# Kernel tuning notes

Measured on AMD Instinct MI355X. Metric: run time of the kernel, lower is better.

Reference implementation:

```python
import jax, jax.numpy as jnp
import numpy as np

BATCH, N_LABELS, HIDDEN, N_EDGES = 2048, 10000, 768, 20000
PENALTY = 1e-4


def setup_inputs() -> dict:
    key = jax.random.key(0)
    k1, k2, k3, k4, k5 = jax.random.split(key, 5)
    logits = jax.random.normal(k1, (BATCH, N_LABELS), dtype=jnp.float32)
    targets = jax.random.uniform(k2, (BATCH, N_LABELS), dtype=jnp.float32)
    params = jax.random.normal(k3, (N_LABELS, HIDDEN), dtype=jnp.float32)
    parent_idx = jax.random.randint(k4, (N_EDGES,), 0, N_LABELS, dtype=jnp.int32)
    child_idx = jax.random.randint(k5, (N_EDGES,), 0, N_LABELS, dtype=jnp.int32)
    return {"logits": logits, "targets": targets, "params": params,
            "parent_idx": parent_idx, "child_idx": child_idx}


def reference(logits, targets, params, parent_idx, child_idx):
    # BCEWithLogitsLoss (mean reduction): softplus(x) - t*x, numerically stable
    bce = jnp.mean(jax.nn.softplus(logits) - targets * logits)
    # recursive regularization: 0.5 * sum_edges ||param[parent] - param[child]||^2
    diff = params[parent_idx] - params[child_idx]  # [E, H] gather-diff
    reg = 0.5 * jnp.sum(diff * diff)
    return bce + PENALTY * reg
```

## Files before the change

kernel.cpp:

```cpp
#include <hip/hip_runtime.h>
#include <hip/hip_bf16.h>

#define BATCH    2048
#define N_LABELS 10000
#define HIDDEN   768
#define N_EDGES  20000
#define PENALTY  1e-4f

constexpr int BCE_THREADS = 256;
constexpr int BCE_BLOCKS  = 2048;
constexpr int REG_THREADS = 256;
constexpr int EDGES_PER_BLOCK = REG_THREADS / 64;
constexpr int REG_BLOCKS  = N_EDGES / EDGES_PER_BLOCK;
constexpr int FIN_THREADS = 1024;

__device__ __forceinline__ float bce_term(float x, float t) {
    float e = __builtin_amdgcn_exp2f(fabsf(x) * -1.44269504f);
    float l = __builtin_amdgcn_logf(1.0f + e);
    return fmaxf(x, 0.0f) + 0.69314718f * l - t * x;
}

__device__ __forceinline__ float wave_reduce(float v) {
#pragma unroll
    for (int o = 32; o > 0; o >>= 1) v += __shfl_down(v, o, 64);
    return v;
}

template <bool USE_ATOMIC>
__global__ void __launch_bounds__(BCE_THREADS)
bce_kernel(const float4* __restrict__ x4, const float4* __restrict__ t4,
           float* __restrict__ dst) {
    const int n4 = (BATCH * N_LABELS) / 4;
    float acc = 0.0f;
    for (int i = blockIdx.x * blockDim.x + threadIdx.x; i < n4;
         i += gridDim.x * blockDim.x) {
        float4 x = x4[i];
        float4 t = t4[i];
        acc += bce_term(x.x, t.x) + bce_term(x.y, t.y) +
               bce_term(x.z, t.z) + bce_term(x.w, t.w);
    }
    acc = wave_reduce(acc);
    __shared__ float s[BCE_THREADS / 64];
    const int lane = threadIdx.x & 63, w = threadIdx.x >> 6;
    if (lane == 0) s[w] = acc;
    __syncthreads();
    if (threadIdx.x == 0) {
        float b = 0.0f;
#pragma unroll
        for (int i = 0; i < BCE_THREADS / 64; ++i) b += s[i];
        b *= (1.0f / ((float)BATCH * (float)N_LABELS));
        if (USE_ATOMIC) atomicAdd(dst, b);
        else            dst[blockIdx.x] = b;
    }
}

template <bool USE_ATOMIC>
__global__ void __launch_bounds__(REG_THREADS)
reg_kernel(const float* __restrict__ params, const int* __restrict__ pidx,
           const int* __restrict__ cidx, float* __restrict__ dst) {
    const int wave = threadIdx.x >> 6;
    const int lane = threadIdx.x & 63;
    const int edge = blockIdx.x * EDGES_PER_BLOCK + wave;

    const int p = pidx[edge];
    const int c = cidx[edge];
    const float4* rp = (const float4*)(params + (size_t)p * HIDDEN);
    const float4* rc = (const float4*)(params + (size_t)c * HIDDEN);

    float acc = 0.0f;
#pragma unroll
    for (int j = 0; j < HIDDEN / 4 / 64; ++j) {
        float4 a = rp[j * 64 + lane];
        float4 b = rc[j * 64 + lane];
        float dx = a.x - b.x, dy = a.y - b.y, dz = a.z - b.z, dw = a.w - b.w;
        acc = fmaf(dx, dx, acc);
        acc = fmaf(dy, dy, acc);
        acc = fmaf(dz, dz, acc);
        acc = fmaf(dw, dw, acc);
    }
    acc = wave_reduce(acc);
    __shared__ float s[EDGES_PER_BLOCK];
    if (lane == 0) s[wave] = acc;
    __syncthreads();
    if (threadIdx.x == 0) {
        float b = 0.0f;
#pragma unroll
        for (int i = 0; i < EDGES_PER_BLOCK; ++i) b += s[i];
        b *= (0.5f * PENALTY);
        if (USE_ATOMIC) atomicAdd(dst, b);
        else            dst[blockIdx.x] = b;
    }
}

__global__ void __launch_bounds__(FIN_THREADS)
finalize_kernel(const float* __restrict__ partials, int n, float* __restrict__ out) {
    float acc = 0.0f;
    for (int i = threadIdx.x; i < n; i += blockDim.x) acc += partials[i];
    acc = wave_reduce(acc);
    __shared__ float s[FIN_THREADS / 64];
    const int lane = threadIdx.x & 63, w = threadIdx.x >> 6;
    if (lane == 0) s[w] = acc;
    __syncthreads();
    if (threadIdx.x == 0) {
        float b = 0.0f;
#pragma unroll
        for (int i = 0; i < FIN_THREADS / 64; ++i) b += s[i];
        out[0] = b;
    }
}

extern "C" void kernel_launch(void* const* d_in, const int* in_sizes, int n_in,
                              void* d_out, int out_size, void* d_ws, size_t ws_size,
                              hipStream_t stream) {
    const float* logits  = (const float*)d_in[0];
    const float* targets = (const float*)d_in[1];
    const float* params  = (const float*)d_in[2];
    const int*   pidx    = (const int*)d_in[3];
    const int*   cidx    = (const int*)d_in[4];
    float* out = (float*)d_out;

    const size_t need = (size_t)(BCE_BLOCKS + REG_BLOCKS) * sizeof(float);
    if (ws_size >= need) {
        float* partials = (float*)d_ws;
        bce_kernel<false><<<BCE_BLOCKS, BCE_THREADS, 0, stream>>>(
            (const float4*)logits, (const float4*)targets, partials);
        reg_kernel<false><<<REG_BLOCKS, REG_THREADS, 0, stream>>>(
            params, pidx, cidx, partials + BCE_BLOCKS);
        finalize_kernel<<<1, FIN_THREADS, 0, stream>>>(partials, BCE_BLOCKS + REG_BLOCKS, out);
    } else {
        hipMemsetAsync(d_out, 0, sizeof(float), stream);
        bce_kernel<true><<<BCE_BLOCKS, BCE_THREADS, 0, stream>>>(
            (const float4*)logits, (const float4*)targets, out);
        reg_kernel<true><<<REG_BLOCKS, REG_THREADS, 0, stream>>>(
            params, pidx, cidx, out);
    }
}
```

Before: 49.31 us.

## Fuse BCE and regularization kernels into one launch with batched loads

```diff
diff --git a/kernel.cpp b/kernel.cpp
--- a/kernel.cpp
+++ b/kernel.cpp
@@ -7,11 +7,14 @@
 #define N_EDGES  20000
 #define PENALTY  1e-4f
 
-constexpr int BCE_THREADS = 256;
-constexpr int BCE_BLOCKS  = 2048;
-constexpr int REG_THREADS = 256;
-constexpr int EDGES_PER_BLOCK = REG_THREADS / 64;
-constexpr int REG_BLOCKS  = N_EDGES / EDGES_PER_BLOCK;
+constexpr int THREADS   = 256;
+constexpr int N4        = BATCH * N_LABELS / 4;
+constexpr int BCE_K     = 10;
+constexpr int BCE_STRIDE = N4 / BCE_K;
+constexpr int BCE_BLOCKS = BCE_STRIDE / THREADS;
+constexpr int EDGES_PER_BLOCK = THREADS / 64;
+constexpr int REG_BLOCKS = N_EDGES / EDGES_PER_BLOCK;
+constexpr int TOTAL_BLOCKS = BCE_BLOCKS + REG_BLOCKS;
 constexpr int FIN_THREADS = 1024;
 
 __device__ __forceinline__ float bce_term(float x, float t) {
@@ -27,68 +30,68 @@
 }
 
 template <bool USE_ATOMIC>
-__global__ void __launch_bounds__(BCE_THREADS)
-bce_kernel(const float4* __restrict__ x4, const float4* __restrict__ t4,
-           float* __restrict__ dst) {
-    const int n4 = (BATCH * N_LABELS) / 4;
-    float acc = 0.0f;
-    for (int i = blockIdx.x * blockDim.x + threadIdx.x; i < n4;
-         i += gridDim.x * blockDim.x) {
-        float4 x = x4[i];
-        float4 t = t4[i];
-        acc += bce_term(x.x, t.x) + bce_term(x.y, t.y) +
-               bce_term(x.z, t.z) + bce_term(x.w, t.w);
-    }
-    acc = wave_reduce(acc);
-    __shared__ float s[BCE_THREADS / 64];
-    const int lane = threadIdx.x & 63, w = threadIdx.x >> 6;
-    if (lane == 0) s[w] = acc;
-    __syncthreads();
-    if (threadIdx.x == 0) {
-        float b = 0.0f;
+__global__ void __launch_bounds__(THREADS)
+fused_kernel(const float4* __restrict__ x4, const float4* __restrict__ t4,
+             const float* __restrict__ params, const int* __restrict__ pidx,
+             const int* __restrict__ cidx, float* __restrict__ dst) {
+    const int lane = threadIdx.x & 63;
+    const int w    = threadIdx.x >> 6;
+    __shared__ float s[THREADS / 64];
+
+    if (blockIdx.x < BCE_BLOCKS) {
+        const int tid = blockIdx.x * THREADS + threadIdx.x;
+        float4 xs[BCE_K], ts[BCE_K];
 #pragma unroll
-        for (int i = 0; i < BCE_THREADS / 64; ++i) b += s[i];
-        b *= (1.0f / ((float)BATCH * (float)N_LABELS));
-        if (USE_ATOMIC) atomicAdd(dst, b);
-        else            dst[blockIdx.x] = b;
-    }
-}
+        for (int j = 0; j < BCE_K; ++j) xs[j] = x4[tid + j * BCE_STRIDE];
+#pragma unroll
+        for (int j = 0; j < BCE_K; ++j) ts[j] = t4[tid + j * BCE_STRIDE];
 
-template <bool USE_ATOMIC>
-__global__ void __launch_bounds__(REG_THREADS)
-reg_kernel(const float* __restrict__ params, const int* __restrict__ pidx,
-           const int* __restrict__ cidx, float* __restrict__ dst) {
-    const int wave = threadIdx.x >> 6;
-    const int lane = threadIdx.x & 63;
-    const int edge = blockIdx.x * EDGES_PER_BLOCK + wave;
+        float acc = 0.0f;
+#pragma unroll
+        for (int j = 0; j < BCE_K; ++j) {
+            acc += bce_term(xs[j].x, ts[j].x) + bce_term(xs[j].y, ts[j].y) +
+                   bce_term(xs[j].z, ts[j].z) + bce_term(xs[j].w, ts[j].w);
+        }
+        acc = wave_reduce(acc);
+        if (lane == 0) s[w] = acc;
+        __syncthreads();
+        if (threadIdx.x == 0) {
+            float b = (s[0] + s[1] + s[2] + s[3]) *
+                      (1.0f / ((float)BATCH * (float)N_LABELS));
+            if (USE_ATOMIC) atomicAdd(dst, b);
+            else            dst[blockIdx.x] = b;
+        }
+    } else {
+        const int edge = (blockIdx.x - BCE_BLOCKS) * EDGES_PER_BLOCK + w;
+        const int p = pidx[edge];
+        const int c = cidx[edge];
+        const float4* rp = (const float4*)(params + (size_t)p * HIDDEN);
+        const float4* rc = (const float4*)(params + (size_t)c * HIDDEN);
 
-    const int p = pidx[edge];
-    const int c = cidx[edge];
-    const float4* rp = (const float4*)(params + (size_t)p * HIDDEN);
-    const float4* rc = (const float4*)(params + (size_t)c * HIDDEN);
+        float4 a[3], b[3];
+#pragma unroll
+        for (int j = 0; j < 3; ++j) a[j] = rp[j * 64 + lane];
+#pragma unroll
+        for (int j = 0; j < 3; ++j) b[j] = rc[j * 64 + lane];
 
-    float acc = 0.0f;
+        float acc = 0.0f;
 #pragma unroll
-    for (int j = 0; j < HIDDEN / 4 / 64; ++j) {
-        float4 a = rp[j * 64 + lane];
-        float4 b = rc[j * 64 + lane];
-        float dx = a.x - b.x, dy = a.y - b.y, dz = a.z - b.z, dw = a.w - b.w;
-        acc = fmaf(dx, dx, acc);
-        acc = fmaf(dy, dy, acc);
-        acc = fmaf(dz, dz, acc);
-        acc = fmaf(dw, dw, acc);
-    }
-    acc = wave_reduce(acc);
-    __shared__ float s[EDGES_PER_BLOCK];
-    if (lane == 0) s[wave] = acc;
-    __syncthreads();
-    if (threadIdx.x == 0) {
-        float b = 0.0f;
-#pragma unroll
-        for (int i = 0; i < EDGES_PER_BLOCK; ++i) b += s[i];
-        b *= (0.5f * PENALTY);
-        if (USE_ATOMIC) atomicAdd(dst, b);
-        else            dst[blockIdx.x] = b;
+        for (int j = 0; j < 3; ++j) {
+            float dx = a[j].x - b[j].x, dy = a[j].y - b[j].y;
+            float dz = a[j].z - b[j].z, dw = a[j].w - b[j].w;
+            acc = fmaf(dx, dx, acc);
+            acc = fmaf(dy, dy, acc);
+            acc = fmaf(dz, dz, acc);
+            acc = fmaf(dw, dw, acc);
+        }
+        acc = wave_reduce(acc);
+        if (lane == 0) s[w] = acc;
+        __syncthreads();
+        if (threadIdx.x == 0) {
+            float b2 = (s[0] + s[1] + s[2] + s[3]) * (0.5f * PENALTY);
+            if (USE_ATOMIC) atomicAdd(dst, b2);
+            else            dst[blockIdx.x] = b2;
+        }
     }
 }
 
@@ -119,19 +122,17 @@
     const int*   cidx    = (const int*)d_in[4];
     float* out = (float*)d_out;
 
-    const size_t need = (size_t)(BCE_BLOCKS + REG_BLOCKS) * sizeof(float);
+    const size_t need = (size_t)TOTAL_BLOCKS * sizeof(float);
     if (ws_size >= need) {
         float* partials = (float*)d_ws;
-        bce_kernel<false><<<BCE_BLOCKS, BCE_THREADS, 0, stream>>>(
-            (const float4*)logits, (const float4*)targets, partials);
-        reg_kernel<false><<<REG_BLOCKS, REG_THREADS, 0, stream>>>(
-            params, pidx, cidx, partials + BCE_BLOCKS);
-        finalize_kernel<<<1, FIN_THREADS, 0, stream>>>(partials, BCE_BLOCKS + REG_BLOCKS, out);
+        fused_kernel<false><<<TOTAL_BLOCKS, THREADS, 0, stream>>>(
+            (const float4*)logits, (const float4*)targets, params, pidx, cidx,
+            partials);
+        finalize_kernel<<<1, FIN_THREADS, 0, stream>>>(partials, TOTAL_BLOCKS, out);
     } else {
         hipMemsetAsync(d_out, 0, sizeof(float), stream);
-        bce_kernel<true><<<BCE_BLOCKS, BCE_THREADS, 0, stream>>>(
-            (const float4*)logits, (const float4*)targets, out);
-        reg_kernel<true><<<REG_BLOCKS, REG_THREADS, 0, stream>>>(
-            params, pidx, cidx, out);
+        fused_kernel<true><<<TOTAL_BLOCKS, THREADS, 0, stream>>>(
+            (const float4*)logits, (const float4*)targets, params, pidx, cidx,
+            out);
     }
 }
```

New measurement: 48.18 us. -2.3%, faster.
